# Kernel optimization log

Measured on AMD Instinct MI355X. Metric: run time of the kernel, lower is better.

The kernel has to match this reference:

```python
import jax, jax.numpy as jnp
import numpy as np

N = 4096      # n_nodes
F = 512       # input_dim
R = 64        # repr_dim
H = 8         # n_heads
EPS_BIAS = 0.01
ALPHA = 0.2   # LeakyReLU negative slope
NEG_BIG = 1e16


def setup_inputs() -> dict:
    key = jax.random.key(0)
    k1, k2, k3, k4, k5 = jax.random.split(key, 5)
    node_matrix = jax.random.normal(k1, (N, F), dtype=jnp.float32)
    adjacency_matrix = (jax.random.uniform(k2, (N, N)) < 0.01).astype(jnp.float32)
    adjacency_matrix = jnp.maximum(adjacency_matrix, jnp.eye(N, dtype=jnp.float32))
    # learned parameters (xavier-ish scale)
    W = jax.random.normal(k3, (H, F, R), dtype=jnp.float32) * 0.06
    shared_attention = jax.random.normal(k4, (H, 2 * R), dtype=jnp.float32) * 0.1
    attention_biases = jax.random.normal(k5, (N, N), dtype=jnp.float32) * 0.02
    return {
        "node_matrix": node_matrix,
        "adjacency_matrix": adjacency_matrix,
        "W": W,
        "shared_attention": shared_attention,
        "attention_biases": attention_biases,
    }


def reference(node_matrix, adjacency_matrix, W, shared_attention, attention_biases):
    # hidden_repr: [H, N, R]
    hidden = jnp.einsum('nf,hfr->hnr', node_matrix, W)
    # per-head source/destination scores: [H, N]
    a_src = jnp.einsum('hnr,hr->hn', hidden, shared_attention[:, :R])
    a_dst = jnp.einsum('hnr,hr->hn', hidden, shared_attention[:, R:])
    # broadcast-sum + trainable pair bias: [H, N, N]
    pre = a_src[:, :, None] + a_dst[:, None, :] + EPS_BIAS * attention_biases[None]
    full = jnp.where(pre >= 0, pre, ALPHA * pre)  # LeakyReLU
    # adjacency masking then row softmax
    scores = full + (-NEG_BIG * (1.0 - adjacency_matrix))[None]
    att = jax.nn.softmax(scores, axis=-1)  # [H, N, N]
    # weighted aggregation: [H, N, R]
    out = jnp.einsum('hnm,hmr->hnr', att, hidden)
    # 'concat' aggregation: [N, H*R], head h occupies columns h*R:(h+1)*R
    return jnp.transpose(out, (1, 0, 2)).reshape(N, H * R)
```

## Files before the change

kernel.cpp:

```cpp
#include <hip/hip_runtime.h>
#include <hip/hip_bf16.h>

#define NN 4096
#define FF 512
#define RR 64
#define HH 8
#define HR (HH * RR)
#define CAP 128
#define ATT_STRIDE 144

typedef short bf16x8 __attribute__((ext_vector_type(8)));
typedef float f32x4 __attribute__((ext_vector_type(4)));

__device__ __forceinline__ unsigned short f2bf(float f) {
  __hip_bfloat16 h = __float2bfloat16(f);
  return *reinterpret_cast<unsigned short*>(&h);
}
__device__ __forceinline__ float bf2f(unsigned short u) {
  union { unsigned u32; float f; } cv;
  cv.u32 = ((unsigned)u) << 16;
  return cv.f;
}
__device__ __forceinline__ unsigned nib4(const float4 v) {
  unsigned m = 0;
  if (v.x != 0.f) m |= 1u;
  if (v.y != 0.f) m |= 2u;
  if (v.z != 0.f) m |= 4u;
  if (v.w != 0.f) m |= 8u;
  return m;
}

__global__ __launch_bounds__(256) void k_convert(
    const float* __restrict__ X, const float* __restrict__ W,
    unsigned short* __restrict__ Xb, unsigned short* __restrict__ BbT)
{
  __shared__ unsigned short wt[64][68];
  const int b = blockIdx.x;
  const int tid = threadIdx.x;

  if (b < 2048) {
    const int t = b * 256 + tid;
    const float4 v = reinterpret_cast<const float4*>(X)[t];
    ushort4 u;
    u.x = f2bf(v.x); u.y = f2bf(v.y); u.z = f2bf(v.z); u.w = f2bf(v.w);
    reinterpret_cast<ushort4*>(Xb)[t] = u;
  } else {
    const int b2 = b - 2048;
    const int h = b2 >> 3;
    const int f0 = (b2 & 7) << 6;
    const int fr = tid >> 2;
    const int rq = (tid & 3) << 4;
    const float* wp = W + (size_t)h * FF * RR + (size_t)(f0 + fr) * RR + rq;
#pragma unroll
    for (int v = 0; v < 4; ++v) {
      const float4 x = *reinterpret_cast<const float4*>(wp + v * 4);
      wt[rq + v * 4 + 0][fr] = f2bf(x.x);
      wt[rq + v * 4 + 1][fr] = f2bf(x.y);
      wt[rq + v * 4 + 2][fr] = f2bf(x.z);
      wt[rq + v * 4 + 3][fr] = f2bf(x.w);
    }
    __syncthreads();
    const int r = tid >> 2;
    unsigned short* op = BbT + (size_t)(h * 64 + r) * FF + f0 + ((tid & 3) << 4);
    int4 w0 = *reinterpret_cast<const int4*>(&wt[r][(tid & 3) << 4]);
    int4 w1 = *reinterpret_cast<const int4*>(&wt[r][((tid & 3) << 4) + 8]);
    *reinterpret_cast<int4*>(op) = w0;
    *reinterpret_cast<int4*>(op + 8) = w1;
  }
}

__global__ __launch_bounds__(256) void k_mega(
    const unsigned short* __restrict__ Xb,
    const unsigned short* __restrict__ BbT,
    const float* __restrict__ sa,
    const float* __restrict__ adj,
    unsigned short* __restrict__ hiddenT,
    float* __restrict__ a_srcT,
    float* __restrict__ a_dstT,
    int* __restrict__ colsG,
    int* __restrict__ cnts)
{
  __shared__ unsigned short Als[64 * 32];
  __shared__ unsigned short Bls[64 * 32];
  __shared__ float redS[64][2];
  __shared__ float redD[64][2];
  const int b = blockIdx.x;
  const int tid = threadIdx.x;

  if (b < 512) {
    const int row0 = (b & 63) * 64;
    const int h = b >> 6;
    const int n0 = h * 64;
    const int l = tid & 63;
    const int wid = tid >> 6;
    const int wr = wid >> 1, wc = wid & 1;

    f32x4 acc[2][2];
#pragma unroll
    for (int a = 0; a < 2; ++a)
#pragma unroll
      for (int bb = 0; bb < 2; ++bb) acc[a][bb] = (f32x4){0.f, 0.f, 0.f, 0.f};

    const int srow = tid >> 2;
    const int skel = (tid & 3) * 8;

    for (int k0 = 0; k0 < FF; k0 += 32) {
      const int4 av = *reinterpret_cast<const int4*>(
          &Xb[(size_t)(row0 + srow) * FF + k0 + skel]);
      const int4 bv = *reinterpret_cast<const int4*>(
          &BbT[(size_t)(n0 + srow) * FF + k0 + skel]);
      __syncthreads();
      *reinterpret_cast<int4*>(&Als[tid * 8]) = av;
      *reinterpret_cast<int4*>(&Bls[tid * 8]) = bv;
      __syncthreads();

      const int ka = (l >> 4) * 8;
      const bf16x8 a0 = *reinterpret_cast<const bf16x8*>(&Als[(32 * wr + 0  + (l & 15)) * 32 + ka]);
      const bf16x8 a1 = *reinterpret_cast<const bf16x8*>(&Als[(32 * wr + 16 + (l & 15)) * 32 + ka]);
      const bf16x8 b0 = *reinterpret_cast<const bf16x8*>(&Bls[(32 * wc + 0  + (l & 15)) * 32 + ka]);
      const bf16x8 b1 = *reinterpret_cast<const bf16x8*>(&Bls[(32 * wc + 16 + (l & 15)) * 32 + ka]);
      acc[0][0] = __builtin_amdgcn_mfma_f32_16x16x32_bf16(a0, b0, acc[0][0], 0, 0, 0);
      acc[0][1] = __builtin_amdgcn_mfma_f32_16x16x32_bf16(a0, b1, acc[0][1], 0, 0, 0);
      acc[1][0] = __builtin_amdgcn_mfma_f32_16x16x32_bf16(a1, b0, acc[1][0], 0, 0, 0);
      acc[1][1] = __builtin_amdgcn_mfma_f32_16x16x32_bf16(a1, b1, acc[1][1], 0, 0, 0);
    }

    const int lg = l >> 4;
    const int lc = l & 15;

#pragma unroll
    for (int mi = 0; mi < 2; ++mi)
#pragma unroll
      for (int ni = 0; ni < 2; ++ni)
#pragma unroll
        for (int j = 0; j < 4; ++j) {
          const int rowg = row0 + 32 * wr + 16 * mi + (lg << 2) + j;
          const int colg = n0 + 32 * wc + 16 * ni + lc;
          hiddenT[(size_t)rowg * HR + colg] = f2bf(acc[mi][ni][j]);
        }

    float sS[2], sD[2];
#pragma unroll
    for (int ni = 0; ni < 2; ++ni) {
      const int col = 32 * wc + 16 * ni + lc;
      sS[ni] = sa[(size_t)h * 2 * RR + col];
      sD[ni] = sa[(size_t)h * 2 * RR + RR + col];
    }
#pragma unroll
    for (int mi = 0; mi < 2; ++mi)
#pragma unroll
      for (int j = 0; j < 4; ++j) {
        float ps = acc[mi][0][j] * sS[0] + acc[mi][1][j] * sS[1];
        float pd = acc[mi][0][j] * sD[0] + acc[mi][1][j] * sD[1];
#pragma unroll
        for (int off = 8; off >= 1; off >>= 1) {
          ps += __shfl_xor(ps, off);
          pd += __shfl_xor(pd, off);
        }
        if (lc == 0) {
          const int rl = 32 * wr + 16 * mi + (lg << 2) + j;
          redS[rl][wc] = ps;
          redD[rl][wc] = pd;
        }
      }
    __syncthreads();
    if (tid < 64) {
      a_srcT[(size_t)(row0 + tid) * HH + h] = redS[tid][0] + redS[tid][1];
      a_dstT[(size_t)(row0 + tid) * HH + h] = redD[tid][0] + redD[tid][1];
    }
  } else {
    const int lane = tid & 63;
    const int row = (b - 512) * 4 + (tid >> 6);
    const float* arow = adj + (size_t)row * NN;
    unsigned long long pm = 0;
    {
      float4 buf[8];
#pragma unroll
      for (int c = 0; c < 8; ++c)
        buf[c] = *reinterpret_cast<const float4*>(&arow[c * 256 + (lane << 2)]);
#pragma unroll
      for (int c = 0; c < 8; ++c)
        pm |= (unsigned long long)nib4(buf[c]) << (4 * c);
#pragma unroll
      for (int c = 0; c < 8; ++c)
        buf[c] = *reinterpret_cast<const float4*>(&arow[(c + 8) * 256 + (lane << 2)]);
#pragma unroll
      for (int c = 0; c < 8; ++c)
        pm |= (unsigned long long)nib4(buf[c]) << (4 * c + 32);
    }
    const int cnt = __popcll(pm);
    int pfx = cnt;
#pragma unroll
    for (int off = 1; off < 64; off <<= 1) {
      const int o = __shfl_up(pfx, off);
      if (lane >= off) pfx += o;
    }
    int pos = pfx - cnt;
    unsigned long long m = pm;
    int* cg = colsG + (size_t)row * CAP;
    while (m) {
      const int bit = (int)__builtin_ctzll(m);
      m &= m - 1;
      if (pos < CAP) cg[pos] = ((bit >> 2) << 8) + (lane << 2) + (bit & 3);
      ++pos;
    }
    const int tot = __shfl(pfx, 63);
    for (int p = tot + lane; p < CAP; p += 64) cg[p] = 0;
    if (lane == 63) cnts[row] = tot < CAP ? tot : CAP;
  }
}

__global__ __launch_bounds__(256) void k_gat_row(
    const int* __restrict__ colsG,
    const int* __restrict__ cnts,
    const float* __restrict__ bias,
    const float* __restrict__ a_srcT,
    const float* __restrict__ a_dstT,
    const unsigned short* __restrict__ hiddenT,
    float* __restrict__ out)
{
  const int i = blockIdx.x;
  const int tid = threadIdx.x;

  __shared__ __align__(16) float att[HH][ATT_STRIDE];
  __shared__ int cols[CAP];
  __shared__ __align__(16) float accred[4][HR];

  int c = 0;
  float4 d0, d1;
  float b = 0.f;
  if (tid < CAP) c = colsG[(size_t)i * CAP + tid];
  const int count = cnts[i];
  if (tid < CAP) {
    b = 0.01f * bias[(size_t)i * NN + c];
    d0 = *reinterpret_cast<const float4*>(&a_dstT[(size_t)c * HH]);
    d1 = *reinterpret_cast<const float4*>(&a_dstT[(size_t)c * HH + 4]);
  }
  const float4 s0 = *reinterpret_cast<const float4*>(&a_srcT[(size_t)i * HH]);
  const float4 s1 = *reinterpret_cast<const float4*>(&a_srcT[(size_t)i * HH + 4]);

  if (tid < CAP) {
    cols[tid] = c;
    float s;
    s = s0.x + d0.x + b; att[0][tid] = (s >= 0.f) ? s : 0.2f * s;
    s = s0.y + d0.y + b; att[1][tid] = (s >= 0.f) ? s : 0.2f * s;
    s = s0.z + d0.z + b; att[2][tid] = (s >= 0.f) ? s : 0.2f * s;
    s = s0.w + d0.w + b; att[3][tid] = (s >= 0.f) ? s : 0.2f * s;
    s = s1.x + d1.x + b; att[4][tid] = (s >= 0.f) ? s : 0.2f * s;
    s = s1.y + d1.y + b; att[5][tid] = (s >= 0.f) ? s : 0.2f * s;
    s = s1.z + d1.z + b; att[6][tid] = (s >= 0.f) ? s : 0.2f * s;
    s = s1.w + d1.w + b; att[7][tid] = (s >= 0.f) ? s : 0.2f * s;
  }
  __syncthreads();

  {
    const int g = tid >> 5;
    const int l = tid & 31;
    float* arow_h = att[g];
    float m = -3.0e38f;
    for (int t = l; t < count; t += 32) m = fmaxf(m, arow_h[t]);
#pragma unroll
    for (int o = 16; o >= 1; o >>= 1) m = fmaxf(m, __shfl_xor(m, o));
    float ssum = 0.f;
    for (int t = l; t < count; t += 32) {
      const float e = expf(arow_h[t] - m);
      arow_h[t] = e;
      ssum += e;
    }
#pragma unroll
    for (int o = 16; o >= 1; o >>= 1) ssum += __shfl_xor(ssum, o);
    const float inv = 1.0f / ssum;
    for (int t = l; t < count; t += 32) arow_h[t] *= inv;
  }
  __syncthreads();

  {
    const int g2 = tid >> 6;
    const int o0 = (tid & 63) << 3;
    const float* attrow = att[o0 >> 6];
    const unsigned short* hb = hiddenT + o0;
    const int q = (count + 3) >> 2;
    const int t0 = g2 * q;
    const int t1 = min(t0 + q, count);
    float4 accA = make_float4(0.f, 0.f, 0.f, 0.f);
    float4 accB = make_float4(0.f, 0.f, 0.f, 0.f);
    for (int t = t0; t < t1; ++t) {
      const int cc = cols[t];
      const float a = attrow[t];
      const ushort4 ua = *reinterpret_cast<const ushort4*>(hb + (size_t)cc * HR);
      const ushort4 ub = *reinterpret_cast<const ushort4*>(hb + (size_t)cc * HR + 4);
      accA.x += a * bf2f(ua.x); accA.y += a * bf2f(ua.y);
      accA.z += a * bf2f(ua.z); accA.w += a * bf2f(ua.w);
      accB.x += a * bf2f(ub.x); accB.y += a * bf2f(ub.y);
      accB.z += a * bf2f(ub.z); accB.w += a * bf2f(ub.w);
    }
    *reinterpret_cast<float4*>(&accred[g2][o0]) = accA;
    *reinterpret_cast<float4*>(&accred[g2][o0 + 4]) = accB;
  }
  __syncthreads();
  {
    const int o = tid << 1;
    const float2 r = make_float2(
        accred[0][o] + accred[1][o] + accred[2][o] + accred[3][o],
        accred[0][o + 1] + accred[1][o + 1] + accred[2][o + 1] + accred[3][o + 1]);
    *reinterpret_cast<float2*>(&out[(size_t)i * HR + o]) = r;
  }
}

extern "C" void kernel_launch(void* const* d_in, const int* in_sizes, int n_in,
                              void* d_out, int out_size, void* d_ws, size_t ws_size,
                              hipStream_t stream) {
  const float* X    = (const float*)d_in[0];
  const float* adj  = (const float*)d_in[1];
  const float* W    = (const float*)d_in[2];
  const float* sa   = (const float*)d_in[3];
  const float* bias = (const float*)d_in[4];
  float* out = (float*)d_out;

  unsigned short* hiddenT = (unsigned short*)d_ws;
  unsigned short* Xb  = hiddenT + (size_t)NN * HR;
  unsigned short* BbT = Xb + (size_t)NN * FF;
  float* a_srcT = (float*)(BbT + (size_t)HR * FF);
  float* a_dstT = a_srcT + (size_t)NN * HH;
  int* cnts     = (int*)(a_dstT + (size_t)NN * HH);
  int* colsG    = cnts + NN;

  k_convert<<<dim3(2112), 256, 0, stream>>>(X, W, Xb, BbT);
  k_mega<<<dim3(1536), 256, 0, stream>>>(Xb, BbT, sa, adj, hiddenT, a_srcT, a_dstT, colsG, cnts);
  k_gat_row<<<dim3(NN), 256, 0, stream>>>(colsG, cnts, bias, a_srcT, a_dstT, hiddenT, out);
}
```

Before: 46.11 us.

## Gather pair bias during adjacency compaction and halve gat_row block size

The compaction pass in k_mega now also gathers the scaled attention bias for each surviving column into a compact per-row buffer. This moves the random bias reads out of the row-aggregation kernel and overlaps them with the GEMM blocks. k_gat_row drops to 128 threads with a two-way split reduction, uses the fast __expf, and pads the attention rows with a smaller stride. The bias gather stays serialized inside the per-lane while loop, and half as many threads now handle the aggregation in each row block.

```diff
diff --git a/kernel.cpp b/kernel.cpp
--- a/kernel.cpp
+++ b/kernel.cpp
@@ -7,7 +7,7 @@
 #define HH 8
 #define HR (HH * RR)
 #define CAP 128
-#define ATT_STRIDE 144
+#define ATT_STRIDE 132
 
 typedef short bf16x8 __attribute__((ext_vector_type(8)));
 typedef float f32x4 __attribute__((ext_vector_type(4)));
@@ -74,10 +74,12 @@
     const unsigned short* __restrict__ BbT,
     const float* __restrict__ sa,
     const float* __restrict__ adj,
+    const float* __restrict__ bias,
     unsigned short* __restrict__ hiddenT,
     float* __restrict__ a_srcT,
     float* __restrict__ a_dstT,
     int* __restrict__ colsG,
+    float* __restrict__ bvalsG,
     int* __restrict__ cnts)
 {
   __shared__ unsigned short Als[64 * 32];
@@ -172,6 +174,7 @@
     const int lane = tid & 63;
     const int row = (b - 512) * 4 + (tid >> 6);
     const float* arow = adj + (size_t)row * NN;
+    const float* brow = bias + (size_t)row * NN;
     unsigned long long pm = 0;
     {
       float4 buf[8];
@@ -198,22 +201,27 @@
     int pos = pfx - cnt;
     unsigned long long m = pm;
     int* cg = colsG + (size_t)row * CAP;
+    float* bg = bvalsG + (size_t)row * CAP;
     while (m) {
       const int bit = (int)__builtin_ctzll(m);
       m &= m - 1;
-      if (pos < CAP) cg[pos] = ((bit >> 2) << 8) + (lane << 2) + (bit & 3);
+      if (pos < CAP) {
+        const int col = ((bit >> 2) << 8) + (lane << 2) + (bit & 3);
+        cg[pos] = col;
+        bg[pos] = 0.01f * brow[col];
+      }
       ++pos;
     }
     const int tot = __shfl(pfx, 63);
-    for (int p = tot + lane; p < CAP; p += 64) cg[p] = 0;
+    for (int p = tot + lane; p < CAP; p += 64) { cg[p] = 0; bg[p] = 0.f; }
     if (lane == 63) cnts[row] = tot < CAP ? tot : CAP;
   }
 }
 
-__global__ __launch_bounds__(256) void k_gat_row(
+__global__ __launch_bounds__(128) void k_gat_row(
     const int* __restrict__ colsG,
+    const float* __restrict__ bvalsG,
     const int* __restrict__ cnts,
-    const float* __restrict__ bias,
     const float* __restrict__ a_srcT,
     const float* __restrict__ a_dstT,
     const unsigned short* __restrict__ hiddenT,
@@ -224,22 +232,17 @@
 
   __shared__ __align__(16) float att[HH][ATT_STRIDE];
   __shared__ int cols[CAP];
-  __shared__ __align__(16) float accred[4][HR];
-
-  int c = 0;
-  float4 d0, d1;
-  float b = 0.f;
-  if (tid < CAP) c = colsG[(size_t)i * CAP + tid];
+  __shared__ __align__(16) float accred[2][HR];
+
+  const int c = colsG[(size_t)i * CAP + tid];
+  const float b = bvalsG[(size_t)i * CAP + tid];
   const int count = cnts[i];
-  if (tid < CAP) {
-    b = 0.01f * bias[(size_t)i * NN + c];
-    d0 = *reinterpret_cast<const float4*>(&a_dstT[(size_t)c * HH]);
-    d1 = *reinterpret_cast<const float4*>(&a_dstT[(size_t)c * HH + 4]);
-  }
+  const float4 d0 = *reinterpret_cast<const float4*>(&a_dstT[(size_t)c * HH]);
+  const float4 d1 = *reinterpret_cast<const float4*>(&a_dstT[(size_t)c * HH + 4]);
   const float4 s0 = *reinterpret_cast<const float4*>(&a_srcT[(size_t)i * HH]);
   const float4 s1 = *reinterpret_cast<const float4*>(&a_srcT[(size_t)i * HH + 4]);
 
-  if (tid < CAP) {
+  {
     cols[tid] = c;
     float s;
     s = s0.x + d0.x + b; att[0][tid] = (s >= 0.f) ? s : 0.2f * s;
@@ -254,23 +257,23 @@
   __syncthreads();
 
   {
-    const int g = tid >> 5;
-    const int l = tid & 31;
+    const int g = tid >> 4;
+    const int l = tid & 15;
     float* arow_h = att[g];
     float m = -3.0e38f;
-    for (int t = l; t < count; t += 32) m = fmaxf(m, arow_h[t]);
-#pragma unroll
-    for (int o = 16; o >= 1; o >>= 1) m = fmaxf(m, __shfl_xor(m, o));
+    for (int t = l; t < count; t += 16) m = fmaxf(m, arow_h[t]);
+#pragma unroll
+    for (int o = 8; o >= 1; o >>= 1) m = fmaxf(m, __shfl_xor(m, o));
     float ssum = 0.f;
-    for (int t = l; t < count; t += 32) {
-      const float e = expf(arow_h[t] - m);
+    for (int t = l; t < count; t += 16) {
+      const float e = __expf(arow_h[t] - m);
       arow_h[t] = e;
       ssum += e;
     }
 #pragma unroll
-    for (int o = 16; o >= 1; o >>= 1) ssum += __shfl_xor(ssum, o);
+    for (int o = 8; o >= 1; o >>= 1) ssum += __shfl_xor(ssum, o);
     const float inv = 1.0f / ssum;
-    for (int t = l; t < count; t += 32) arow_h[t] *= inv;
+    for (int t = l; t < count; t += 16) arow_h[t] *= inv;
   }
   __syncthreads();
 
@@ -279,9 +282,9 @@
     const int o0 = (tid & 63) << 3;
     const float* attrow = att[o0 >> 6];
     const unsigned short* hb = hiddenT + o0;
-    const int q = (count + 3) >> 2;
-    const int t0 = g2 * q;
-    const int t1 = min(t0 + q, count);
+    const int half = (count + 1) >> 1;
+    const int t0 = g2 * half;
+    const int t1 = min(t0 + half, count);
     float4 accA = make_float4(0.f, 0.f, 0.f, 0.f);
     float4 accB = make_float4(0.f, 0.f, 0.f, 0.f);
     for (int t = t0; t < t1; ++t) {
@@ -299,11 +302,11 @@
   }
   __syncthreads();
   {
-    const int o = tid << 1;
-    const float2 r = make_float2(
-        accred[0][o] + accred[1][o] + accred[2][o] + accred[3][o],
-        accred[0][o + 1] + accred[1][o + 1] + accred[2][o + 1] + accred[3][o + 1]);
-    *reinterpret_cast<float2*>(&out[(size_t)i * HR + o]) = r;
+    const int o = tid << 2;
+    const float4 v0 = *reinterpret_cast<const float4*>(&accred[0][o]);
+    const float4 v1 = *reinterpret_cast<const float4*>(&accred[1][o]);
+    const float4 r = make_float4(v0.x + v1.x, v0.y + v1.y, v0.z + v1.z, v0.w + v1.w);
+    *reinterpret_cast<float4*>(&out[(size_t)i * HR + o]) = r;
   }
 }
 
@@ -324,8 +327,10 @@
   float* a_dstT = a_srcT + (size_t)NN * HH;
   int* cnts     = (int*)(a_dstT + (size_t)NN * HH);
   int* colsG    = cnts + NN;
+  float* bvalsG = (float*)(colsG + (size_t)NN * CAP);
 
   k_convert<<<dim3(2112), 256, 0, stream>>>(X, W, Xb, BbT);
-  k_mega<<<dim3(1536), 256, 0, stream>>>(Xb, BbT, sa, adj, hiddenT, a_srcT, a_dstT, colsG, cnts);
-  k_gat_row<<<dim3(NN), 256, 0, stream>>>(colsG, cnts, bias, a_srcT, a_dstT, hiddenT, out);
-}
+  k_mega<<<dim3(1536), 256, 0, stream>>>(Xb, BbT, sa, adj, bias, hiddenT,
+                                         a_srcT, a_dstT, colsG, bvalsG, cnts);
+  k_gat_row<<<dim3(NN), 128, 0, stream>>>(colsG, bvalsG, cnts, a_srcT, a_dstT, hiddenT, out);
+}
```

Measured after the change: 44.32 us (median of 2 runs). 3.9% less time.
